# Kernel tuning notes

Measured on AMD Instinct MI355X. Metric: run time of the kernel, lower is better.

## Reference

```python
import jax, jax.numpy as jnp
import numpy as np

D_OUT = 1536
BN_EPS = 1e-5


def _batchnorm(h, g, b):
    # torch BatchNorm1d in training mode: biased batch stats
    m = jnp.mean(h, axis=0)
    v = jnp.var(h, axis=0)
    return g * (h - m) * jax.lax.rsqrt(v + BN_EPS) + b


def setup_inputs() -> dict:
    key = jax.random.key(0)
    ks = jax.random.split(key, 16)
    B = 8192
    d0, d1, dib = 1024, 768, 1024
    s = lambda d: (2.0 / d) ** 0.5
    inp = {
        "x0": jax.random.normal(ks[0], (B, d0), jnp.float32),
        "x1": jax.random.normal(ks[1], (B, d1), jnp.float32),
        "x_ib": jax.random.normal(ks[2], (B, dib), jnp.float32),
        # 7 expert projections per source (Reaction_Head_mini modeled as linear proj)
        "pW0": jax.random.normal(ks[3], (7, d0, D_OUT), jnp.float32) * s(d0),
        "pb0": jnp.zeros((7, D_OUT), jnp.float32),
        "pW1": jax.random.normal(ks[4], (7, d1, D_OUT), jnp.float32) * s(d1),
        "pb1": jnp.zeros((7, D_OUT), jnp.float32),
        "pWib": jax.random.normal(ks[5], (7, dib, D_OUT), jnp.float32) * s(dib),
        "pbib": jnp.zeros((7, D_OUT), jnp.float32),
        # MOE_Router_Sig: Linear(1024,512)+BN+relu -> Linear(512,100)+BN+tanh -> Linear(100,3)
        "rw1": jax.random.normal(ks[6], (d0, 512), jnp.float32) * s(d0),
        "rb1": jnp.zeros((512,), jnp.float32),
        "rg1": jnp.ones((512,), jnp.float32),
        "rbt1": jnp.zeros((512,), jnp.float32),
        "rw2": jax.random.normal(ks[7], (512, 100), jnp.float32) * s(512),
        "rb2": jnp.zeros((100,), jnp.float32),
        "rg2": jnp.ones((100,), jnp.float32),
        "rbt2": jnp.zeros((100,), jnp.float32),
        "rw3": jax.random.normal(ks[8], (100, 3), jnp.float32) * s(100),
        "rb3": jnp.zeros((3,), jnp.float32),
    }
    return inp


def reference(x0, x1, x_ib, pW0, pb0, pW1, pb1, pWib, pbib,
              rw1, rb1, rg1, rbt1, rw2, rb2, rg2, rbt2, rw3, rb3):
    # ---- expert projections (torch.no_grad in original) ----
    e0 = jnp.einsum('bd,kdf->bkf', x0, pW0) + pb0      # [B,7,1536]
    e1 = jnp.einsum('bd,kdf->bkf', x1, pW1) + pb1      # [B,7,1536]
    eib = jnp.einsum('bd,kdf->bkf', x_ib, pWib) + pbib # [B,7,1536]
    ex = jnp.concatenate([e0, e1, eib], axis=1)        # [B,21,1536]
    B = ex.shape[0]
    # seg_mean with segment length 7 -> [B,3,1536]
    ex = ex.reshape(B, 3, 7, D_OUT).mean(axis=2)
    ex = jax.lax.stop_gradient(ex)
    # ---- router: MOE_Router_Sig(x0) -> sigmoid -> softmax ----
    h = _batchnorm(x0 @ rw1 + rb1, rg1, rbt1)
    h = jax.nn.relu(h)
    h = _batchnorm(h @ rw2 + rb2, rg2, rbt2)
    h = jnp.tanh(h)
    logits = jax.nn.sigmoid(h @ rw3 + rb3)             # [B,3]
    w = jax.nn.softmax(logits, axis=-1)                # [B,3]
    # ---- weighted combine + L2 normalize ----
    out = jnp.sum(ex * w[:, :, None], axis=1)          # [B,1536]
    out = out / jnp.linalg.norm(out, axis=-1, keepdims=True).clip(1e-12)
    return out
```

## Files before the change

kernel.cpp:

```cpp
#include <hip/hip_runtime.h>
#include <stdint.h>

typedef __attribute__((ext_vector_type(8))) short short8;
typedef __attribute__((ext_vector_type(4))) float floatx4;

__device__ inline unsigned short f2bf(float f) {
    unsigned int u = __float_as_uint(f);
    u += 0x7fffu + ((u >> 16) & 1u);
    return (unsigned short)(u >> 16);
}

__device__ void avg_transpose_tile(const float* __restrict__ src,
                                   unsigned short* __restrict__ dst,
                                   int E, int K, int Nsrc, int Ndst, int ldb,
                                   float scale, int tile_x, int tile_y) {
    __shared__ float tile[32][33];
    const int tid = threadIdx.x;
    const int tx = tid & 31;
    const int ty = tid >> 5;
    const int kb = tile_x * 32;
    const int nb = tile_y * 32;
#pragma unroll
    for (int p = 0; p < 4; ++p) {
        int kl = ty + p * 8;
        int k = kb + kl;
        int n = nb + tx;
        float s = 0.f;
        if (k < K && n < Nsrc) {
            for (int e = 0; e < E; ++e)
                s += src[(size_t)e * K * Nsrc + (size_t)k * Nsrc + n];
        }
        tile[kl][tx] = s * scale;
    }
    __syncthreads();
#pragma unroll
    for (int p = 0; p < 4; ++p) {
        int nl = ty + p * 8;
        int n = nb + nl;
        int k = kb + tx;
        if (n < Ndst && k < K)
            dst[(size_t)n * ldb + k] = f2bf(tile[tx][nl]);
    }
}

__global__ __launch_bounds__(256) void prep(
    const float* __restrict__ pW0, const float* __restrict__ pW1,
    const float* __restrict__ pWib, const float* __restrict__ rw1,
    const float* __restrict__ rw2, const float* __restrict__ pb0,
    const float* __restrict__ pb1, const float* __restrict__ pbib,
    const float* __restrict__ x0,
    unsigned short* __restrict__ Wmt, unsigned short* __restrict__ rw1t,
    unsigned short* __restrict__ rw2t, float* __restrict__ bm0,
    float* __restrict__ bm1, float* __restrict__ bm2,
    float* __restrict__ stats_zero, unsigned short* __restrict__ X0b) {
    int id = blockIdx.x;
    int tid = threadIdx.x;
    if (id < 1536) {
        avg_transpose_tile(pW0, Wmt + 0, 7, 1024, 1536, 1536, 2816, 1.f / 7.f,
                           id % 32, id / 32);
    } else if (id < 2688) {
        int t = id - 1536;
        avg_transpose_tile(pW1, Wmt + 1024, 7, 768, 1536, 1536, 2816, 1.f / 7.f,
                           t % 24, t / 24);
    } else if (id < 4224) {
        int t = id - 2688;
        avg_transpose_tile(pWib, Wmt + 1792, 7, 1024, 1536, 1536, 2816,
                           1.f / 7.f, t % 32, t / 32);
    } else if (id < 4736) {
        int t = id - 4224;
        avg_transpose_tile(rw1, rw1t, 1, 1024, 512, 512, 1024, 1.f, t % 32,
                           t / 32);
    } else if (id < 4800) {
        int t = id - 4736;
        avg_transpose_tile(rw2, rw2t, 1, 512, 100, 128, 512, 1.f, t % 16,
                           t / 16);
    } else if (id < 4806) {
        int i = (id - 4800) * 256 + tid;
        if (i < 1536) {
            float s0 = 0.f, s1 = 0.f, s2 = 0.f;
            for (int e = 0; e < 7; ++e) {
                s0 += pb0[e * 1536 + i];
                s1 += pb1[e * 1536 + i];
                s2 += pbib[e * 1536 + i];
            }
            const float inv = 1.f / 7.f;
            bm0[i] = s0 * inv; bm1[i] = s1 * inv; bm2[i] = s2 * inv;
        }
    } else if (id < 4807) {
        for (int i = tid; i < 1280; i += 256) stats_zero[i] = 0.f;
    } else {
        int base = (id - 4807) * 1024;
#pragma unroll
        for (int k = 0; k < 4; ++k) {
            int i = base + k * 256 + tid;
            float4 v = ((const float4*)x0)[i];
            ushort4 o;
            o.x = f2bf(v.x); o.y = f2bf(v.y); o.z = f2bf(v.z); o.w = f2bf(v.w);
            ((ushort4*)X0b)[i] = o;
        }
    }
}

template <int MODE>
__global__ __launch_bounds__(256) void gemm_bt(
    const unsigned short* __restrict__ A, const unsigned short* __restrict__ Bt,
    float* __restrict__ C, int K, int Nreal, int ldc,
    const float* __restrict__ bias, float* __restrict__ sum,
    float* __restrict__ sumsq, const float* __restrict__ w0,
    const float* __restrict__ w1, const float* __restrict__ w2,
    const float* __restrict__ bm0, const float* __restrict__ bm1,
    const float* __restrict__ bm2) {
    __shared__ __align__(16) unsigned short As[128 * 32];
    __shared__ __align__(16) unsigned short Bs[128 * 32];
    const int tid = threadIdx.x;
    const int lane = tid & 63;
    const int wv = tid >> 6;
    const int bm_off = blockIdx.x * 128;
    const int bn_off = blockIdx.y * 128;
    const int wm = (wv & 1) * 64;
    const int wn = (wv >> 1) * 64;
    floatx4 acc[4][4];
#pragma unroll
    for (int i = 0; i < 4; ++i)
#pragma unroll
        for (int j = 0; j < 4; ++j) acc[i][j] = (floatx4){0.f, 0.f, 0.f, 0.f};

    const int quad = lane >> 4;
    const int lrow = lane & 15;
    const int srow = lane >> 2;
    const int scol = (lane & 3) * 8;

    const unsigned short* Ag = A + (size_t)bm_off * K;
    const unsigned short* Bg = Bt + (size_t)bn_off * K;

    for (int k0 = 0; k0 < K; k0 += 32) {
#pragma unroll
        for (int r = 0; r < 2; ++r) {
            int chunk = r * 4 + wv;
            {
                const unsigned short* gp =
                    Ag + (size_t)(chunk * 16 + srow) * K + (k0 + scol);
                __builtin_amdgcn_global_load_lds(
                    (const __attribute__((address_space(1))) void*)gp,
                    (__attribute__((address_space(3))) void*)(As + chunk * 512),
                    16, 0, 0);
            }
            {
                const unsigned short* gp =
                    Bg + (size_t)(chunk * 16 + srow) * K + (k0 + scol);
                __builtin_amdgcn_global_load_lds(
                    (const __attribute__((address_space(1))) void*)gp,
                    (__attribute__((address_space(3))) void*)(Bs + chunk * 512),
                    16, 0, 0);
            }
        }
        __syncthreads();
        short8 af[4], bfr[4];
#pragma unroll
        for (int i = 0; i < 4; ++i)
            af[i] = *(const short8*)(As + (wm + i * 16 + lrow) * 32 + quad * 8);
#pragma unroll
        for (int j = 0; j < 4; ++j)
            bfr[j] = *(const short8*)(Bs + (wn + j * 16 + lrow) * 32 + quad * 8);
#pragma unroll
        for (int i = 0; i < 4; ++i)
#pragma unroll
            for (int j = 0; j < 4; ++j)
                acc[i][j] = __builtin_amdgcn_mfma_f32_16x16x32_bf16(
                    af[i], bfr[j], acc[i][j], 0, 0, 0);
        __syncthreads();
    }

    if (MODE == 1) {
#pragma unroll
        for (int i = 0; i < 4; ++i) {
#pragma unroll
            for (int r = 0; r < 4; ++r) {
                int m = bm_off + wm + i * 16 + quad * 4 + r;
                float wb0 = w0[m], wb1 = w1[m], wb2 = w2[m];
#pragma unroll
                for (int j = 0; j < 4; ++j) {
                    int n = bn_off + wn + j * 16 + lrow;
                    float v = acc[i][j][r] + wb0 * bm0[n] + wb1 * bm1[n] +
                              wb2 * bm2[n];
                    C[(size_t)m * ldc + n] = v;
                }
            }
        }
    } else {
#pragma unroll
        for (int j = 0; j < 4; ++j) {
            int n = bn_off + wn + j * 16 + lrow;
            bool nok = (n < Nreal);
            float bv = nok ? bias[n] : 0.f;
            float s = 0.f, ss = 0.f;
#pragma unroll
            for (int i = 0; i < 4; ++i) {
#pragma unroll
                for (int r = 0; r < 4; ++r) {
                    float v = acc[i][j][r] + bv;
                    int m = bm_off + wm + i * 16 + quad * 4 + r;
                    if (nok) C[(size_t)m * ldc + n] = v;
                    s += v; ss += v * v;
                }
            }
            s += __shfl_xor(s, 16); s += __shfl_xor(s, 32);
            ss += __shfl_xor(ss, 16); ss += __shfl_xor(ss, 32);
            if (quad == 0 && nok) {
                atomicAdd(&sum[n], s);
                atomicAdd(&sumsq[n], ss);
            }
        }
    }
}

__global__ __launch_bounds__(256) void bn_relu_pack(
    const float* __restrict__ h, unsigned short* __restrict__ out,
    const float* __restrict__ sum, const float* __restrict__ sumsq,
    const float* __restrict__ g, const float* __restrict__ b) {
    __shared__ float sc[512], sh[512];
    const float invB = 1.f / 8192.f;
    for (int c = threadIdx.x; c < 512; c += 256) {
        float m = sum[c] * invB;
        float v = sumsq[c] * invB - m * m;
        float s = g[c] * rsqrtf(v + 1e-5f);
        sc[c] = s;
        sh[c] = b[c] - m * s;
    }
    __syncthreads();
    int base = blockIdx.x * 4096;
#pragma unroll
    for (int k = 0; k < 16; ++k) {
        int i = base + k * 256 + threadIdx.x;
        int c4 = (i & 127) * 4;
        float4 v = ((const float4*)h)[i];
        ushort4 o;
        o.x = f2bf(fmaxf(v.x * sc[c4 + 0] + sh[c4 + 0], 0.f));
        o.y = f2bf(fmaxf(v.y * sc[c4 + 1] + sh[c4 + 1], 0.f));
        o.z = f2bf(fmaxf(v.z * sc[c4 + 2] + sh[c4 + 2], 0.f));
        o.w = f2bf(fmaxf(v.w * sc[c4 + 3] + sh[c4 + 3], 0.f));
        ((ushort4*)out)[i] = o;
    }
}

__global__ __launch_bounds__(128) void router_tail(
    const float* __restrict__ h2, const float* __restrict__ sum,
    const float* __restrict__ sumsq, const float* __restrict__ g,
    const float* __restrict__ b, const float* __restrict__ rw3,
    const float* __restrict__ rb3, float* __restrict__ w0,
    float* __restrict__ w1, float* __restrict__ w2) {
    __shared__ float sc[100], sh[100], w3[300], b3[3];
    int tid = threadIdx.x;
    const float invB = 1.f / 8192.f;
    if (tid < 100) {
        float m = sum[tid] * invB;
        float v = sumsq[tid] * invB - m * m;
        float s = g[tid] * rsqrtf(v + 1e-5f);
        sc[tid] = s;
        sh[tid] = b[tid] - m * s;
    }
    for (int i = tid; i < 300; i += 128) w3[i] = rw3[i];
    if (tid < 3) b3[tid] = rb3[tid];
    __syncthreads();
    int bi = blockIdx.x * 128 + tid;
    float l0 = b3[0], l1 = b3[1], l2 = b3[2];
    const float* hr = h2 + (size_t)bi * 100;
    for (int k = 0; k < 100; ++k) {
        float t = tanhf(hr[k] * sc[k] + sh[k]);
        l0 += t * w3[k * 3 + 0];
        l1 += t * w3[k * 3 + 1];
        l2 += t * w3[k * 3 + 2];
    }
    l0 = 1.f / (1.f + expf(-l0));
    l1 = 1.f / (1.f + expf(-l1));
    l2 = 1.f / (1.f + expf(-l2));
    float mx = fmaxf(l0, fmaxf(l1, l2));
    float e0 = expf(l0 - mx), e1 = expf(l1 - mx), e2 = expf(l2 - mx);
    float inv = 1.f / (e0 + e1 + e2);
    w0[bi] = e0 * inv; w1[bi] = e1 * inv; w2[bi] = e2 * inv;
}

__global__ __launch_bounds__(256) void pack_xp(
    const float* __restrict__ x0, const float* __restrict__ x1,
    const float* __restrict__ xib, const float* __restrict__ w0,
    const float* __restrict__ w1, const float* __restrict__ w2,
    unsigned short* __restrict__ Xp) {
    int i = blockIdx.x * blockDim.x + threadIdx.x;
    if (i >= 8192 * 704) return;
    int b = i / 704;
    int g = i % 704;
    const float* src;
    float w;
    int col;
    if (g < 256)      { src = x0 + (size_t)b * 1024 + g * 4;          w = w0[b]; col = g * 4; }
    else if (g < 448) { src = x1 + (size_t)b * 768 + (g - 256) * 4;   w = w1[b]; col = 1024 + (g - 256) * 4; }
    else              { src = xib + (size_t)b * 1024 + (g - 448) * 4; w = w2[b]; col = 1792 + (g - 448) * 4; }
    float4 v = *(const float4*)src;
    ushort4 o;
    o.x = f2bf(v.x * w); o.y = f2bf(v.y * w);
    o.z = f2bf(v.z * w); o.w = f2bf(v.w * w);
    *(ushort4*)(Xp + (size_t)b * 2816 + col) = o;
}

__global__ __launch_bounds__(256) void l2norm_rows(float* __restrict__ out) {
    int wv = threadIdx.x >> 6;
    int lane = threadIdx.x & 63;
    int row = blockIdx.x * 4 + wv;
    float4* rp = (float4*)(out + (size_t)row * 1536);
    float4 v[6];
    float ss = 0.f;
#pragma unroll
    for (int t = 0; t < 6; ++t) {
        v[t] = rp[lane + t * 64];
        ss += v[t].x * v[t].x + v[t].y * v[t].y + v[t].z * v[t].z + v[t].w * v[t].w;
    }
#pragma unroll
    for (int o = 32; o > 0; o >>= 1) ss += __shfl_xor(ss, o);
    float inv = 1.f / fmaxf(sqrtf(ss), 1e-12f);
#pragma unroll
    for (int t = 0; t < 6; ++t) {
        v[t].x *= inv; v[t].y *= inv; v[t].z *= inv; v[t].w *= inv;
        rp[lane + t * 64] = v[t];
    }
}

extern "C" void kernel_launch(void* const* d_in, const int* in_sizes, int n_in,
                              void* d_out, int out_size, void* d_ws,
                              size_t ws_size, hipStream_t stream) {
    (void)in_sizes; (void)n_in; (void)out_size; (void)ws_size;
    const float* x0   = (const float*)d_in[0];
    const float* x1   = (const float*)d_in[1];
    const float* xib  = (const float*)d_in[2];
    const float* pW0  = (const float*)d_in[3];
    const float* pb0  = (const float*)d_in[4];
    const float* pW1  = (const float*)d_in[5];
    const float* pb1  = (const float*)d_in[6];
    const float* pWib = (const float*)d_in[7];
    const float* pbib = (const float*)d_in[8];
    const float* rw1  = (const float*)d_in[9];
    const float* rb1  = (const float*)d_in[10];
    const float* rg1  = (const float*)d_in[11];
    const float* rbt1 = (const float*)d_in[12];
    const float* rw2  = (const float*)d_in[13];
    const float* rb2  = (const float*)d_in[14];
    const float* rg2  = (const float*)d_in[15];
    const float* rbt2 = (const float*)d_in[16];
    const float* rw3  = (const float*)d_in[17];
    const float* rb3  = (const float*)d_in[18];
    float* out = (float*)d_out;

    char* ws = (char*)d_ws;
    unsigned short* Wmt = (unsigned short*)(ws);
    char* stats = ws + 8650752;
    float* sum1   = (float*)(stats + 0);
    float* sumsq1 = (float*)(stats + 2048);
    float* sum2   = (float*)(stats + 4096);
    float* sumsq2 = (float*)(stats + 4608);
    float* bm0    = (float*)(stats + 10240);
    float* bm1    = (float*)(stats + 16384);
    float* bm2    = (float*)(stats + 22528);
    float* w0p    = (float*)(stats + 28672);
    float* w1p    = (float*)(stats + 61440);
    float* w2p    = (float*)(stats + 94208);
    unsigned short* rw1t = (unsigned short*)(ws + 8781824);
    unsigned short* rw2t = (unsigned short*)(ws + 9830400);
    char* R5 = ws + 9961472;
    unsigned short* X0b = (unsigned short*)(R5);
    float* h1           = (float*)(R5 + 16777216);
    unsigned short* h1n = (unsigned short*)(R5 + 33554432);
    float* h2           = (float*)(R5 + 41943040);
    unsigned short* Xp  = (unsigned short*)(R5);

    prep<<<6855, 256, 0, stream>>>(pW0, pW1, pWib, rw1, rw2, pb0, pb1, pbib, x0,
                                   Wmt, rw1t, rw2t, bm0, bm1, bm2,
                                   (float*)stats, X0b);
    gemm_bt<2><<<dim3(64, 4), 256, 0, stream>>>(
        X0b, rw1t, h1, 1024, 512, 512, rb1, sum1, sumsq1,
        nullptr, nullptr, nullptr, nullptr, nullptr, nullptr);
    bn_relu_pack<<<256, 256, 0, stream>>>(h1, h1n, sum1, sumsq1, rg1, rbt1);
    gemm_bt<2><<<dim3(64, 1), 256, 0, stream>>>(
        h1n, rw2t, h2, 512, 100, 100, rb2, sum2, sumsq2,
        nullptr, nullptr, nullptr, nullptr, nullptr, nullptr);
    router_tail<<<64, 128, 0, stream>>>(h2, sum2, sumsq2, rg2, rbt2, rw3, rb3,
                                        w0p, w1p, w2p);
    pack_xp<<<22528, 256, 0, stream>>>(x0, x1, xib, w0p, w1p, w2p, Xp);
    gemm_bt<1><<<dim3(64, 12), 256, 0, stream>>>(
        Xp, Wmt, out, 2816, 1536, 1536, nullptr, nullptr, nullptr,
        w0p, w1p, w2p, bm0, bm1, bm2);
    l2norm_rows<<<2048, 256, 0, stream>>>(out);
}
```

Before: 484.5 us.

## Fuse router into cooperative kernel and fold routing weights into GEMM accumulator

Packs all three inputs to unweighted bf16 once in prep, so x0 is converted only once and the separate weighted pack kernel goes away. The router's two GEMMs, batchnorms and tail now run in one cooperative kernel with grid syncs, so h1 is never stored in fp32. The final GEMM applies routing weights by rescaling the accumulator between K segments, using ratios w0/w1 and w1/w2, and then multiplies by w2. This can lose precision or overflow when a weight is tiny, and the grid syncs and the 256-block cooperative launch have their own costs.

```diff
diff --git a/kernel.cpp b/kernel.cpp
--- a/kernel.cpp
+++ b/kernel.cpp
@@ -1,5 +1,8 @@
 #include <hip/hip_runtime.h>
+#include <hip/hip_cooperative_groups.h>
 #include <stdint.h>
+
+namespace cg = cooperative_groups;
 
 typedef __attribute__((ext_vector_type(8))) short short8;
 typedef __attribute__((ext_vector_type(4))) float floatx4;
@@ -48,11 +51,12 @@
     const float* __restrict__ pWib, const float* __restrict__ rw1,
     const float* __restrict__ rw2, const float* __restrict__ pb0,
     const float* __restrict__ pb1, const float* __restrict__ pbib,
-    const float* __restrict__ x0,
+    const float* __restrict__ x0, const float* __restrict__ x1,
+    const float* __restrict__ xib,
     unsigned short* __restrict__ Wmt, unsigned short* __restrict__ rw1t,
     unsigned short* __restrict__ rw2t, float* __restrict__ bm0,
     float* __restrict__ bm1, float* __restrict__ bm2,
-    float* __restrict__ stats_zero, unsigned short* __restrict__ X0b) {
+    float* __restrict__ stats_zero, unsigned short* __restrict__ Xp) {
     int id = blockIdx.x;
     int tid = threadIdx.x;
     if (id < 1536) {
@@ -93,66 +97,50 @@
 #pragma unroll
         for (int k = 0; k < 4; ++k) {
             int i = base + k * 256 + tid;
-            float4 v = ((const float4*)x0)[i];
+            int b = i / 704;
+            int g = i % 704;
+            const float* src;
+            int col;
+            if (g < 256)      { src = x0 + (size_t)b * 1024 + g * 4;          col = g * 4; }
+            else if (g < 448) { src = x1 + (size_t)b * 768 + (g - 256) * 4;   col = 1024 + (g - 256) * 4; }
+            else              { src = xib + (size_t)b * 1024 + (g - 448) * 4; col = 1792 + (g - 448) * 4; }
+            float4 v = *(const float4*)src;
             ushort4 o;
             o.x = f2bf(v.x); o.y = f2bf(v.y); o.z = f2bf(v.z); o.w = f2bf(v.w);
-            ((ushort4*)X0b)[i] = o;
-        }
-    }
-}
-
-template <int MODE>
-__global__ __launch_bounds__(256) void gemm_bt(
-    const unsigned short* __restrict__ A, const unsigned short* __restrict__ Bt,
-    float* __restrict__ C, int K, int Nreal, int ldc,
-    const float* __restrict__ bias, float* __restrict__ sum,
-    float* __restrict__ sumsq, const float* __restrict__ w0,
-    const float* __restrict__ w1, const float* __restrict__ w2,
-    const float* __restrict__ bm0, const float* __restrict__ bm1,
-    const float* __restrict__ bm2) {
-    __shared__ __align__(16) unsigned short As[128 * 32];
-    __shared__ __align__(16) unsigned short Bs[128 * 32];
+            *(ushort4*)(Xp + (size_t)b * 2816 + col) = o;
+        }
+    }
+}
+
+__device__ __forceinline__ void gemm_core(
+    floatx4 (&acc)[4][4], const unsigned short* __restrict__ A, int lda,
+    const unsigned short* __restrict__ Bt, int ldb, int K,
+    unsigned short* As, unsigned short* Bs) {
     const int tid = threadIdx.x;
     const int lane = tid & 63;
     const int wv = tid >> 6;
-    const int bm_off = blockIdx.x * 128;
-    const int bn_off = blockIdx.y * 128;
     const int wm = (wv & 1) * 64;
     const int wn = (wv >> 1) * 64;
-    floatx4 acc[4][4];
-#pragma unroll
-    for (int i = 0; i < 4; ++i)
-#pragma unroll
-        for (int j = 0; j < 4; ++j) acc[i][j] = (floatx4){0.f, 0.f, 0.f, 0.f};
-
     const int quad = lane >> 4;
     const int lrow = lane & 15;
     const int srow = lane >> 2;
     const int scol = (lane & 3) * 8;
-
-    const unsigned short* Ag = A + (size_t)bm_off * K;
-    const unsigned short* Bg = Bt + (size_t)bn_off * K;
-
     for (int k0 = 0; k0 < K; k0 += 32) {
 #pragma unroll
         for (int r = 0; r < 2; ++r) {
             int chunk = r * 4 + wv;
-            {
-                const unsigned short* gp =
-                    Ag + (size_t)(chunk * 16 + srow) * K + (k0 + scol);
-                __builtin_amdgcn_global_load_lds(
-                    (const __attribute__((address_space(1))) void*)gp,
-                    (__attribute__((address_space(3))) void*)(As + chunk * 512),
-                    16, 0, 0);
-            }
-            {
-                const unsigned short* gp =
-                    Bg + (size_t)(chunk * 16 + srow) * K + (k0 + scol);
-                __builtin_amdgcn_global_load_lds(
-                    (const __attribute__((address_space(1))) void*)gp,
-                    (__attribute__((address_space(3))) void*)(Bs + chunk * 512),
-                    16, 0, 0);
-            }
+            const unsigned short* ga =
+                A + (size_t)(chunk * 16 + srow) * lda + (k0 + scol);
+            __builtin_amdgcn_global_load_lds(
+                (const __attribute__((address_space(1))) void*)ga,
+                (__attribute__((address_space(3))) void*)(As + chunk * 512),
+                16, 0, 0);
+            const unsigned short* gb =
+                Bt + (size_t)(chunk * 16 + srow) * ldb + (k0 + scol);
+            __builtin_amdgcn_global_load_lds(
+                (const __attribute__((address_space(1))) void*)gb,
+                (__attribute__((address_space(3))) void*)(Bs + chunk * 512),
+                16, 0, 0);
         }
         __syncthreads();
         short8 af[4], bfr[4];
@@ -170,136 +158,216 @@
                     af[i], bfr[j], acc[i][j], 0, 0, 0);
         __syncthreads();
     }
-
-    if (MODE == 1) {
-#pragma unroll
-        for (int i = 0; i < 4; ++i) {
-#pragma unroll
-            for (int r = 0; r < 4; ++r) {
-                int m = bm_off + wm + i * 16 + quad * 4 + r;
-                float wb0 = w0[m], wb1 = w1[m], wb2 = w2[m];
-#pragma unroll
-                for (int j = 0; j < 4; ++j) {
-                    int n = bn_off + wn + j * 16 + lrow;
-                    float v = acc[i][j][r] + wb0 * bm0[n] + wb1 * bm1[n] +
-                              wb2 * bm2[n];
-                    C[(size_t)m * ldc + n] = v;
-                }
-            }
-        }
-    } else {
+}
+
+__global__ __launch_bounds__(256) void router_mega(
+    const unsigned short* __restrict__ Xp,
+    const unsigned short* __restrict__ rw1t,
+    const unsigned short* __restrict__ rw2t, unsigned short* __restrict__ h1n,
+    float* __restrict__ h2, const float* __restrict__ rb1,
+    const float* __restrict__ rg1, const float* __restrict__ rbt1,
+    const float* __restrict__ rb2, const float* __restrict__ rg2,
+    const float* __restrict__ rbt2, const float* __restrict__ rw3,
+    const float* __restrict__ rb3, float* __restrict__ sum1,
+    float* __restrict__ sumsq1, float* __restrict__ sum2,
+    float* __restrict__ sumsq2, float* __restrict__ r01,
+    float* __restrict__ r12, float* __restrict__ w0p, float* __restrict__ w1p,
+    float* __restrict__ w2p) {
+    __shared__ __align__(16) unsigned short As[4096];
+    __shared__ __align__(16) unsigned short Bs[4096];
+    cg::grid_group grid = cg::this_grid();
+    const int tid = threadIdx.x;
+    const int lane = tid & 63;
+    const int wv = tid >> 6;
+    const int wm = (wv & 1) * 64;
+    const int wn = (wv >> 1) * 64;
+    const int quad = lane >> 4;
+    const int lrow = lane & 15;
+    const int bid = blockIdx.x;
+    const float invB = 1.f / 8192.f;
+
+    {
+        const int bm_off = (bid & 63) * 128;
+        const int bn_off = (bid >> 6) * 128;
+        floatx4 acc[4][4];
+#pragma unroll
+        for (int i = 0; i < 4; ++i)
+#pragma unroll
+            for (int j = 0; j < 4; ++j) acc[i][j] = (floatx4){0.f, 0.f, 0.f, 0.f};
+        gemm_core(acc, Xp + (size_t)bm_off * 2816, 2816,
+                  rw1t + (size_t)bn_off * 1024, 1024, 1024, As, Bs);
 #pragma unroll
         for (int j = 0; j < 4; ++j) {
             int n = bn_off + wn + j * 16 + lrow;
-            bool nok = (n < Nreal);
-            float bv = nok ? bias[n] : 0.f;
+            float bv = rb1[n];
             float s = 0.f, ss = 0.f;
 #pragma unroll
-            for (int i = 0; i < 4; ++i) {
+            for (int i = 0; i < 4; ++i)
 #pragma unroll
                 for (int r = 0; r < 4; ++r) {
                     float v = acc[i][j][r] + bv;
-                    int m = bm_off + wm + i * 16 + quad * 4 + r;
-                    if (nok) C[(size_t)m * ldc + n] = v;
                     s += v; ss += v * v;
                 }
-            }
             s += __shfl_xor(s, 16); s += __shfl_xor(s, 32);
             ss += __shfl_xor(ss, 16); ss += __shfl_xor(ss, 32);
-            if (quad == 0 && nok) {
-                atomicAdd(&sum[n], s);
-                atomicAdd(&sumsq[n], ss);
+            if (quad == 0) { atomicAdd(&sum1[n], s); atomicAdd(&sumsq1[n], ss); }
+        }
+        __threadfence();
+        grid.sync();
+        __threadfence();
+#pragma unroll
+        for (int j = 0; j < 4; ++j) {
+            int n = bn_off + wn + j * 16 + lrow;
+            float bv = rb1[n];
+            float mu = sum1[n] * invB;
+            float var = sumsq1[n] * invB - mu * mu;
+            float sc = rg1[n] * rsqrtf(var + 1e-5f);
+            float sh = rbt1[n] - mu * sc;
+#pragma unroll
+            for (int i = 0; i < 4; ++i)
+#pragma unroll
+                for (int r = 0; r < 4; ++r) {
+                    int mm = bm_off + wm + i * 16 + quad * 4 + r;
+                    float v = acc[i][j][r] + bv;
+                    float t = fmaxf(v * sc + sh, 0.f);
+                    h1n[(size_t)mm * 512 + n] = f2bf(t);
+                }
+        }
+    }
+    __threadfence();
+    grid.sync();
+    __threadfence();
+
+    if (bid < 64) {
+        const int bm_off = bid * 128;
+        floatx4 acc[4][4];
+#pragma unroll
+        for (int i = 0; i < 4; ++i)
+#pragma unroll
+            for (int j = 0; j < 4; ++j) acc[i][j] = (floatx4){0.f, 0.f, 0.f, 0.f};
+        gemm_core(acc, h1n + (size_t)bm_off * 512, 512, rw2t, 512, 512, As, Bs);
+#pragma unroll
+        for (int j = 0; j < 4; ++j) {
+            int n = wn + j * 16 + lrow;
+            bool nok = (n < 100);
+            float bv = nok ? rb2[n] : 0.f;
+            float s = 0.f, ss = 0.f;
+#pragma unroll
+            for (int i = 0; i < 4; ++i)
+#pragma unroll
+                for (int r = 0; r < 4; ++r) {
+                    float v = acc[i][j][r] + bv;
+                    int mm = bm_off + wm + i * 16 + quad * 4 + r;
+                    if (nok) h2[(size_t)mm * 100 + n] = v;
+                    s += v; ss += v * v;
+                }
+            s += __shfl_xor(s, 16); s += __shfl_xor(s, 32);
+            ss += __shfl_xor(ss, 16); ss += __shfl_xor(ss, 32);
+            if (quad == 0 && nok) { atomicAdd(&sum2[n], s); atomicAdd(&sumsq2[n], ss); }
+        }
+    }
+    __threadfence();
+    grid.sync();
+    __threadfence();
+
+    if (bid < 32) {
+        float* scf = (float*)As;
+        float* shf = scf + 128;
+        float* w3  = (float*)Bs;
+        float* b3  = w3 + 304;
+        if (tid < 100) {
+            float mu = sum2[tid] * invB;
+            float var = sumsq2[tid] * invB - mu * mu;
+            float s = rg2[tid] * rsqrtf(var + 1e-5f);
+            scf[tid] = s;
+            shf[tid] = rbt2[tid] - mu * s;
+        }
+        for (int i = tid; i < 300; i += 256) w3[i] = rw3[i];
+        if (tid < 3) b3[tid] = rb3[tid];
+        __syncthreads();
+        int row = bid * 256 + tid;
+        const float* hr = h2 + (size_t)row * 100;
+        float l0 = b3[0], l1 = b3[1], l2 = b3[2];
+        for (int k = 0; k < 100; ++k) {
+            float t = tanhf(hr[k] * scf[k] + shf[k]);
+            l0 += t * w3[k * 3 + 0];
+            l1 += t * w3[k * 3 + 1];
+            l2 += t * w3[k * 3 + 2];
+        }
+        l0 = 1.f / (1.f + expf(-l0));
+        l1 = 1.f / (1.f + expf(-l1));
+        l2 = 1.f / (1.f + expf(-l2));
+        float mx = fmaxf(l0, fmaxf(l1, l2));
+        float e0 = expf(l0 - mx), e1 = expf(l1 - mx), e2 = expf(l2 - mx);
+        float inv = 1.f / (e0 + e1 + e2);
+        w0p[row] = e0 * inv;
+        w1p[row] = e1 * inv;
+        w2p[row] = e2 * inv;
+        r01[row] = e0 / e1;
+        r12[row] = e1 / e2;
+    }
+}
+
+__global__ __launch_bounds__(256, 3) void gemm_final(
+    const unsigned short* __restrict__ Xp, const unsigned short* __restrict__ Wmt,
+    float* __restrict__ C, const float* __restrict__ r01,
+    const float* __restrict__ r12, const float* __restrict__ w0p,
+    const float* __restrict__ w1p, const float* __restrict__ w2p,
+    const float* __restrict__ bm0, const float* __restrict__ bm1,
+    const float* __restrict__ bm2) {
+    __shared__ __align__(16) unsigned short As[4096];
+    __shared__ __align__(16) unsigned short Bs[4096];
+    const int tid = threadIdx.x;
+    const int lane = tid & 63;
+    const int wv = tid >> 6;
+    const int wm = (wv & 1) * 64;
+    const int wn = (wv >> 1) * 64;
+    const int quad = lane >> 4;
+    const int lrow = lane & 15;
+    const int bm_off = blockIdx.x * 128;
+    const int bn_off = blockIdx.y * 128;
+    floatx4 acc[4][4];
+#pragma unroll
+    for (int i = 0; i < 4; ++i)
+#pragma unroll
+        for (int j = 0; j < 4; ++j) acc[i][j] = (floatx4){0.f, 0.f, 0.f, 0.f};
+
+    const unsigned short* Ab = Xp + (size_t)bm_off * 2816;
+    const unsigned short* Bb = Wmt + (size_t)bn_off * 2816;
+
+    gemm_core(acc, Ab, 2816, Bb, 2816, 1024, As, Bs);
+#pragma unroll
+    for (int i = 0; i < 4; ++i)
+#pragma unroll
+        for (int r = 0; r < 4; ++r) {
+            float f = r01[bm_off + wm + i * 16 + quad * 4 + r];
+#pragma unroll
+            for (int j = 0; j < 4; ++j) acc[i][j][r] *= f;
+        }
+    gemm_core(acc, Ab + 1024, 2816, Bb + 1024, 2816, 768, As, Bs);
+#pragma unroll
+    for (int i = 0; i < 4; ++i)
+#pragma unroll
+        for (int r = 0; r < 4; ++r) {
+            float f = r12[bm_off + wm + i * 16 + quad * 4 + r];
+#pragma unroll
+            for (int j = 0; j < 4; ++j) acc[i][j][r] *= f;
+        }
+    gemm_core(acc, Ab + 1792, 2816, Bb + 1792, 2816, 1024, As, Bs);
+
+#pragma unroll
+    for (int i = 0; i < 4; ++i)
+#pragma unroll
+        for (int r = 0; r < 4; ++r) {
+            int m = bm_off + wm + i * 16 + quad * 4 + r;
+            float a0 = w0p[m], a1 = w1p[m], a2 = w2p[m];
+#pragma unroll
+            for (int j = 0; j < 4; ++j) {
+                int n = bn_off + wn + j * 16 + lrow;
+                C[(size_t)m * 1536 + n] =
+                    a2 * acc[i][j][r] + a0 * bm0[n] + a1 * bm1[n] + a2 * bm2[n];
             }
         }
-    }
-}
-
-__global__ __launch_bounds__(256) void bn_relu_pack(
-    const float* __restrict__ h, unsigned short* __restrict__ out,
-    const float* __restrict__ sum, const float* __restrict__ sumsq,
-    const float* __restrict__ g, const float* __restrict__ b) {
-    __shared__ float sc[512], sh[512];
-    const float invB = 1.f / 8192.f;
-    for (int c = threadIdx.x; c < 512; c += 256) {
-        float m = sum[c] * invB;
-        float v = sumsq[c] * invB - m * m;
-        float s = g[c] * rsqrtf(v + 1e-5f);
-        sc[c] = s;
-        sh[c] = b[c] - m * s;
-    }
-    __syncthreads();
-    int base = blockIdx.x * 4096;
-#pragma unroll
-    for (int k = 0; k < 16; ++k) {
-        int i = base + k * 256 + threadIdx.x;
-        int c4 = (i & 127) * 4;
-        float4 v = ((const float4*)h)[i];
-        ushort4 o;
-        o.x = f2bf(fmaxf(v.x * sc[c4 + 0] + sh[c4 + 0], 0.f));
-        o.y = f2bf(fmaxf(v.y * sc[c4 + 1] + sh[c4 + 1], 0.f));
-        o.z = f2bf(fmaxf(v.z * sc[c4 + 2] + sh[c4 + 2], 0.f));
-        o.w = f2bf(fmaxf(v.w * sc[c4 + 3] + sh[c4 + 3], 0.f));
-        ((ushort4*)out)[i] = o;
-    }
-}
-
-__global__ __launch_bounds__(128) void router_tail(
-    const float* __restrict__ h2, const float* __restrict__ sum,
-    const float* __restrict__ sumsq, const float* __restrict__ g,
-    const float* __restrict__ b, const float* __restrict__ rw3,
-    const float* __restrict__ rb3, float* __restrict__ w0,
-    float* __restrict__ w1, float* __restrict__ w2) {
-    __shared__ float sc[100], sh[100], w3[300], b3[3];
-    int tid = threadIdx.x;
-    const float invB = 1.f / 8192.f;
-    if (tid < 100) {
-        float m = sum[tid] * invB;
-        float v = sumsq[tid] * invB - m * m;
-        float s = g[tid] * rsqrtf(v + 1e-5f);
-        sc[tid] = s;
-        sh[tid] = b[tid] - m * s;
-    }
-    for (int i = tid; i < 300; i += 128) w3[i] = rw3[i];
-    if (tid < 3) b3[tid] = rb3[tid];
-    __syncthreads();
-    int bi = blockIdx.x * 128 + tid;
-    float l0 = b3[0], l1 = b3[1], l2 = b3[2];
-    const float* hr = h2 + (size_t)bi * 100;
-    for (int k = 0; k < 100; ++k) {
-        float t = tanhf(hr[k] * sc[k] + sh[k]);
-        l0 += t * w3[k * 3 + 0];
-        l1 += t * w3[k * 3 + 1];
-        l2 += t * w3[k * 3 + 2];
-    }
-    l0 = 1.f / (1.f + expf(-l0));
-    l1 = 1.f / (1.f + expf(-l1));
-    l2 = 1.f / (1.f + expf(-l2));
-    float mx = fmaxf(l0, fmaxf(l1, l2));
-    float e0 = expf(l0 - mx), e1 = expf(l1 - mx), e2 = expf(l2 - mx);
-    float inv = 1.f / (e0 + e1 + e2);
-    w0[bi] = e0 * inv; w1[bi] = e1 * inv; w2[bi] = e2 * inv;
-}
-
-__global__ __launch_bounds__(256) void pack_xp(
-    const float* __restrict__ x0, const float* __restrict__ x1,
-    const float* __restrict__ xib, const float* __restrict__ w0,
-    const float* __restrict__ w1, const float* __restrict__ w2,
-    unsigned short* __restrict__ Xp) {
-    int i = blockIdx.x * blockDim.x + threadIdx.x;
-    if (i >= 8192 * 704) return;
-    int b = i / 704;
-    int g = i % 704;
-    const float* src;
-    float w;
-    int col;
-    if (g < 256)      { src = x0 + (size_t)b * 1024 + g * 4;          w = w0[b]; col = g * 4; }
-    else if (g < 448) { src = x1 + (size_t)b * 768 + (g - 256) * 4;   w = w1[b]; col = 1024 + (g - 256) * 4; }
-    else              { src = xib + (size_t)b * 1024 + (g - 448) * 4; w = w2[b]; col = 1792 + (g - 448) * 4; }
-    float4 v = *(const float4*)src;
-    ushort4 o;
-    o.x = f2bf(v.x * w); o.y = f2bf(v.y * w);
-    o.z = f2bf(v.z * w); o.w = f2bf(v.w * w);
-    *(ushort4*)(Xp + (size_t)b * 2816 + col) = o;
 }
 
 __global__ __launch_bounds__(256) void l2norm_rows(float* __restrict__ out) {
@@ -351,41 +419,40 @@
 
     char* ws = (char*)d_ws;
     unsigned short* Wmt = (unsigned short*)(ws);
-    char* stats = ws + 8650752;
-    float* sum1   = (float*)(stats + 0);
-    float* sumsq1 = (float*)(stats + 2048);
-    float* sum2   = (float*)(stats + 4096);
-    float* sumsq2 = (float*)(stats + 4608);
-    float* bm0    = (float*)(stats + 10240);
-    float* bm1    = (float*)(stats + 16384);
-    float* bm2    = (float*)(stats + 22528);
-    float* w0p    = (float*)(stats + 28672);
-    float* w1p    = (float*)(stats + 61440);
-    float* w2p    = (float*)(stats + 94208);
-    unsigned short* rw1t = (unsigned short*)(ws + 8781824);
-    unsigned short* rw2t = (unsigned short*)(ws + 9830400);
-    char* R5 = ws + 9961472;
-    unsigned short* X0b = (unsigned short*)(R5);
-    float* h1           = (float*)(R5 + 16777216);
-    unsigned short* h1n = (unsigned short*)(R5 + 33554432);
-    float* h2           = (float*)(R5 + 41943040);
-    unsigned short* Xp  = (unsigned short*)(R5);
-
-    prep<<<6855, 256, 0, stream>>>(pW0, pW1, pWib, rw1, rw2, pb0, pb1, pbib, x0,
-                                   Wmt, rw1t, rw2t, bm0, bm1, bm2,
-                                   (float*)stats, X0b);
-    gemm_bt<2><<<dim3(64, 4), 256, 0, stream>>>(
-        X0b, rw1t, h1, 1024, 512, 512, rb1, sum1, sumsq1,
-        nullptr, nullptr, nullptr, nullptr, nullptr, nullptr);
-    bn_relu_pack<<<256, 256, 0, stream>>>(h1, h1n, sum1, sumsq1, rg1, rbt1);
-    gemm_bt<2><<<dim3(64, 1), 256, 0, stream>>>(
-        h1n, rw2t, h2, 512, 100, 100, rb2, sum2, sumsq2,
-        nullptr, nullptr, nullptr, nullptr, nullptr, nullptr);
-    router_tail<<<64, 128, 0, stream>>>(h2, sum2, sumsq2, rg2, rbt2, rw3, rb3,
-                                        w0p, w1p, w2p);
-    pack_xp<<<22528, 256, 0, stream>>>(x0, x1, xib, w0p, w1p, w2p, Xp);
-    gemm_bt<1><<<dim3(64, 12), 256, 0, stream>>>(
-        Xp, Wmt, out, 2816, 1536, 1536, nullptr, nullptr, nullptr,
-        w0p, w1p, w2p, bm0, bm1, bm2);
+    char* S = ws + 8650752;
+    float* sum1   = (float*)(S + 0);
+    float* sumsq1 = (float*)(S + 2048);
+    float* sum2   = (float*)(S + 4096);
+    float* sumsq2 = (float*)(S + 4608);
+    float* bm0    = (float*)(S + 5120);
+    float* bm1    = (float*)(S + 11264);
+    float* bm2    = (float*)(S + 17408);
+    float* w0p    = (float*)(S + 23552);
+    float* w1p    = (float*)(S + 56320);
+    float* w2p    = (float*)(S + 89088);
+    float* r01    = (float*)(S + 121856);
+    float* r12    = (float*)(S + 154624);
+    unsigned short* rw1t = (unsigned short*)(ws + 8838144);
+    unsigned short* rw2t = (unsigned short*)(ws + 9886720);
+    char* R = ws + 10017792;
+    unsigned short* Xp  = (unsigned short*)(R);
+    unsigned short* h1n = (unsigned short*)(R + 46137344);
+    float* h2           = (float*)(R + 54525952);
+
+    prep<<<10439, 256, 0, stream>>>(pW0, pW1, pWib, rw1, rw2, pb0, pb1, pbib,
+                                    x0, x1, xib, Wmt, rw1t, rw2t, bm0, bm1,
+                                    bm2, (float*)S, Xp);
+    {
+        void* args[] = {(void*)&Xp,  (void*)&rw1t, (void*)&rw2t, (void*)&h1n,
+                        (void*)&h2,  (void*)&rb1,  (void*)&rg1,  (void*)&rbt1,
+                        (void*)&rb2, (void*)&rg2,  (void*)&rbt2, (void*)&rw3,
+                        (void*)&rb3, (void*)&sum1, (void*)&sumsq1,
+                        (void*)&sum2, (void*)&sumsq2, (void*)&r01, (void*)&r12,
+                        (void*)&w0p, (void*)&w1p, (void*)&w2p};
+        hipLaunchCooperativeKernel((void*)router_mega, dim3(256), dim3(256),
+                                   args, 0, stream);
+    }
+    gemm_final<<<dim3(64, 12), 256, 0, stream>>>(Xp, Wmt, out, r01, r12, w0p,
+                                                 w1p, w2p, bm0, bm1, bm2);
     l2norm_rows<<<2048, 256, 0, stream>>>(out);
 }
```

After: 665.9 us. +37.4%, slower.
